# Optimization experiments

Measured on AMD Instinct MI355X. Metric: run time of the kernel, lower is better.

Reference implementation:

```python
import jax, jax.numpy as jnp
import numpy as np

D_MODEL = 1024
NUM_HEADS = 16
D_K = D_MODEL // NUM_HEADS
NEG = jnp.float32(-1e9)  # finite stand-in for -inf to keep softmax NaN-free on fully masked rows


def setup_inputs() -> dict:
    key = jax.random.key(0)
    ks = jax.random.split(key, 7)
    B, N_q, N_kv = 2, 2048, 2048
    x = jax.random.normal(ks[0], (B, N_q, D_MODEL), dtype=jnp.float32)
    K = jax.random.normal(ks[1], (B, NUM_HEADS, N_kv, D_K), dtype=jnp.float32)
    V = jax.random.normal(ks[2], (B, NUM_HEADS, N_kv, D_K), dtype=jnp.float32)
    # pad masks: True = keep. Ensure first kv position is always valid.
    kv_pad_mask = jax.random.uniform(ks[3], (B, 1, 1, N_kv)) > 0.1
    kv_pad_mask = kv_pad_mask.at[..., 0].set(True)
    q_pad_mask = jax.random.uniform(ks[4], (B, 1, N_q, 1)) > 0.1
    # params (torch Linear, bias=False); stored as [in, out] so y = x @ W
    Wq = jax.random.normal(ks[5], (D_MODEL, D_MODEL), dtype=jnp.float32) / np.sqrt(D_MODEL)
    Wo = jax.random.normal(ks[6], (D_MODEL, D_MODEL), dtype=jnp.float32) / np.sqrt(D_MODEL)
    return {"x": x, "K": K, "V": V, "Wq": Wq, "Wo": Wo,
            "kv_pad_mask": kv_pad_mask, "q_pad_mask": q_pad_mask}


def reference(x, K, V, Wq, Wo, kv_pad_mask, q_pad_mask):
    B, N_q, D = x.shape
    H, d_k = NUM_HEADS, D_K
    # Q projection and split into heads: [B, H, N_q, d_k]
    Q = (x @ Wq).reshape(B, N_q, H, d_k).transpose(0, 2, 1, 3)
    scores = jnp.einsum('bhqd,bhkd->bhqk', Q, K) / np.sqrt(d_k).astype(np.float32)
    keep = q_pad_mask & kv_pad_mask  # broadcast to [B,1,N_q,N_kv]
    scores = jnp.where(keep, scores, NEG)
    probs = jax.nn.softmax(scores, axis=-1)
    attn = jnp.einsum('bhqk,bhkd->bhqd', probs, V)  # [B,H,N_q,d_k]
    attn = attn.transpose(0, 2, 1, 3).reshape(B, N_q, H * d_k)
    return attn @ Wo
```

## Files before the change

kernel.cpp:

```cpp
#include <hip/hip_runtime.h>
#include <hip/hip_bf16.h>
#include <stdint.h>

typedef __hip_bfloat16 bf16;
typedef __attribute__((ext_vector_type(8))) short short8;
typedef __attribute__((ext_vector_type(4))) short s16x4;
typedef __attribute__((ext_vector_type(4))) float floatx4;

#define MFMA16(a, b, c) __builtin_amdgcn_mfma_f32_16x16x32_bf16(a, b, c, 0, 0, 0)

__device__ __forceinline__ void async_lds16(const void* g, void* l) {
  __builtin_amdgcn_global_load_lds((__attribute__((address_space(1))) const void*)g,
                                   (__attribute__((address_space(3))) void*)l, 16, 0, 0);
}

__device__ __forceinline__ unsigned rne2(float a, float b) {
  unsigned ua = __float_as_uint(a), ub = __float_as_uint(b);
  ua = ua + 0x7FFFu + ((ua >> 16) & 1u);
  ub = ub + 0x7FFFu + ((ub >> 16) & 1u);
  return (ua >> 16) | (ub & 0xFFFF0000u);
}

__global__ __launch_bounds__(256) void prep_k(const float* __restrict__ x, bf16* __restrict__ xb,
                                              const float* __restrict__ Kf, bf16* __restrict__ Kb,
                                              const float* __restrict__ Wq, bf16* __restrict__ WqT,
                                              const float* __restrict__ Wo, bf16* __restrict__ WoT,
                                              const float* __restrict__ V, bf16* __restrict__ VTb,
                                              const int* __restrict__ kvm, const int* __restrict__ qm,
                                              float* __restrict__ kvB, float* __restrict__ qB) {
  __shared__ float tile[64][65];
  int bid = blockIdx.x, tid = threadIdx.x;
  if (bid < 8192) {
    const float* s; bf16* d; int g = bid;
    if (g < 4096) { s = x; d = xb; } else { s = Kf; d = Kb; g -= 4096; }
    int i = (g * 256 + tid) * 4;
    float4 v = *(const float4*)(s + i);
    uint2 o = {rne2(v.x, v.y), rne2(v.z, v.w)};
    *(uint2*)(d + i) = o;
    return;
  }
  if (bid < 9744 - 16) {
    const float* s; bf16* d; int r0, c0, R, C;
    if (bid < 8704) {
      int idx = bid - 8192;
      s = (idx >> 8) ? Wo : Wq; d = (idx >> 8) ? WoT : WqT;
      int rem = idx & 255;
      r0 = (rem & 15) * 64; c0 = (rem >> 4) * 64; R = 1024; C = 1024;
    } else {
      int idx = bid - 8704;
      int m = idx >> 5;
      s = V + (size_t)m * 2048 * 64; d = VTb + (size_t)m * 2048 * 64;
      r0 = (idx & 31) * 64; c0 = 0; R = 2048; C = 64;
    }
    int tr = tid >> 2, tg = tid & 3;
#pragma unroll
    for (int k = 0; k < 4; ++k) {
      int col = tg * 16 + k * 4;
      float4 v = *(const float4*)(s + (size_t)(r0 + tr) * C + c0 + col);
      tile[tr][col] = v.x; tile[tr][col + 1] = v.y;
      tile[tr][col + 2] = v.z; tile[tr][col + 3] = v.w;
    }
    __syncthreads();
    int orow = tid >> 2, ch = tid & 3;
    bf16* drow = d + (size_t)(c0 + orow) * R + r0;
    uint4 w0, w1;
    w0.x = rne2(tile[ch * 8 + 0][orow], tile[ch * 8 + 1][orow]);
    w0.y = rne2(tile[ch * 8 + 2][orow], tile[ch * 8 + 3][orow]);
    w0.z = rne2(tile[ch * 8 + 4][orow], tile[ch * 8 + 5][orow]);
    w0.w = rne2(tile[ch * 8 + 6][orow], tile[ch * 8 + 7][orow]);
    w1.x = rne2(tile[32 + ch * 8 + 0][orow], tile[32 + ch * 8 + 1][orow]);
    w1.y = rne2(tile[32 + ch * 8 + 2][orow], tile[32 + ch * 8 + 3][orow]);
    w1.z = rne2(tile[32 + ch * 8 + 4][orow], tile[32 + ch * 8 + 5][orow]);
    w1.w = rne2(tile[32 + ch * 8 + 6][orow], tile[32 + ch * 8 + 7][orow]);
    *(uint4*)(drow + ch * 8) = w0;
    *(uint4*)(drow + 32 + ch * 8) = w1;
    return;
  }
  int i = (bid - (9744 - 16)) * 256 + tid;
  kvB[i] = kvm[i] ? 0.0f : -3000.0f;
  qB[i]  = qm[i]  ? 0.0f : -3000.0f;
}

__device__ __forceinline__ void storeC(bf16* C, size_t i, float v) { C[i] = __float2bfloat16(v); }
__device__ __forceinline__ void storeC(float* C, size_t i, float v) { C[i] = v; }

template <typename OT>
__global__ __launch_bounds__(256) void gemm_bt_k(const bf16* __restrict__ A,
                                                 const bf16* __restrict__ BT,
                                                 OT* __restrict__ C,
                                                 int M, int N, int K, float scale) {
  __shared__ __align__(16) bf16 As[64 * 64];
  __shared__ __align__(16) bf16 Bs[64 * 64];
  int tid = threadIdx.x;
  int wave = tid >> 6, lane = tid & 63;
  int quad = lane >> 4, lm = lane & 15;
  int wm = wave >> 1, wn = wave & 1;
  int row0 = blockIdx.y * 64, col0 = blockIdx.x * 64;

  floatx4 acc[2][2];
#pragma unroll
  for (int mt = 0; mt < 2; ++mt)
#pragma unroll
    for (int nt = 0; nt < 2; ++nt) acc[mt][nt] = (floatx4){0.f, 0.f, 0.f, 0.f};

  for (int k0 = 0; k0 < K; k0 += 64) {
    __syncthreads();
#pragma unroll
    for (int ch = 0; ch < 2; ++ch) {
      int e = (wave * 2 + ch) * 512 + lane * 8;
      int r = e >> 6, c16 = (e & 63) >> 3;
      int sc = (c16 ^ (r & 7)) * 8;
      async_lds16(A + (size_t)(row0 + r) * K + k0 + sc, &As[(wave * 2 + ch) * 512]);
    }
#pragma unroll
    for (int ch = 0; ch < 2; ++ch) {
      int e = (wave * 2 + ch) * 512 + lane * 8;
      int r = e >> 6, c16 = (e & 63) >> 3;
      int sc = (c16 ^ (r & 7)) * 8;
      async_lds16(BT + (size_t)(col0 + r) * K + k0 + sc, &Bs[(wave * 2 + ch) * 512]);
    }
    __syncthreads();
    int sw = lm & 7;
#pragma unroll
    for (int ks = 0; ks < 64; ks += 32) {
      short8 af[2], bfr[2];
#pragma unroll
      for (int mt = 0; mt < 2; ++mt) {
        int R = wm * 32 + mt * 16 + lm;
        af[mt] = *(const short8*)&As[R * 64 + ((((ks >> 3) + quad) ^ sw) * 8)];
      }
#pragma unroll
      for (int nt = 0; nt < 2; ++nt) {
        int R = wn * 32 + nt * 16 + lm;
        bfr[nt] = *(const short8*)&Bs[R * 64 + ((((ks >> 3) + quad) ^ sw) * 8)];
      }
#pragma unroll
      for (int mt = 0; mt < 2; ++mt)
#pragma unroll
        for (int nt = 0; nt < 2; ++nt)
          acc[mt][nt] = MFMA16(af[mt], bfr[nt], acc[mt][nt]);
    }
  }
#pragma unroll
  for (int mt = 0; mt < 2; ++mt)
#pragma unroll
    for (int nt = 0; nt < 2; ++nt)
#pragma unroll
      for (int j = 0; j < 4; ++j) {
        int rr = row0 + wm * 32 + mt * 16 + quad * 4 + j;
        int cc = col0 + wn * 32 + nt * 16 + lm;
        storeC(C, (size_t)rr * N + cc, acc[mt][nt][j] * scale);
      }
}

__global__ __launch_bounds__(256, 4) void attn_k(const bf16* __restrict__ Q,
                                                 const bf16* __restrict__ Km,
                                                 const bf16* __restrict__ VT,
                                                 const float* __restrict__ qB,
                                                 const float* __restrict__ kvB,
                                                 bf16* __restrict__ O) {
  const float TINY = 9.313225746154785e-10f;
  __shared__ __align__(16) bf16 Ks[64 * 64];
  __shared__ __align__(16) bf16 Vs[64 * 64];
  __shared__ __align__(16) float kvBs[2048];

  int tid = threadIdx.x;
  int wave = tid >> 6, lane = tid & 63;
  int quad = lane >> 4, lm = lane & 15;
  int qb = blockIdx.x, h = blockIdx.y, b = blockIdx.z;
  int q0 = qb * 64 + wave * 16;

  const bf16* kbase = Km + (size_t)(b * 16 + h) * 2048 * 64;
  const bf16* vbase = VT + (size_t)(b * 16 + h) * 64 * 2048;
  const float* kvBb = kvB + b * 2048;

#pragma unroll
  for (int c = 0; c < 2; ++c)
    async_lds16(kvBb + (wave * 2 + c) * 256 + lane * 4, &kvBs[(wave * 2 + c) * 256]);

  short8 aq0, aq1;
  float qbias;
  {
    const bf16* qp = Q + (size_t)(b * 2048 + q0 + lm) * 1024 + h * 64 + quad * 8;
    aq0 = *(const short8*)qp;
    aq1 = *(const short8*)(qp + 32);
    qbias = qB[b * 2048 + q0 + lm];
  }

  short8 ones;
#pragma unroll
  for (int i = 0; i < 8; ++i) ones[i] = (short)0x3F80;

  floatx4 o_acc[4];
  floatx4 l_acc = (floatx4){0.f, 0.f, 0.f, 0.f};
#pragma unroll
  for (int t = 0; t < 4; ++t) o_acc[t] = (floatx4){0.f, 0.f, 0.f, 0.f};

  union S8U { short8 s8; s16x4 h[2]; unsigned u[4]; };

  for (int kv0 = 0; kv0 < 2048; kv0 += 64) {
    __syncthreads();
#pragma unroll
    for (int c = 0; c < 2; ++c) {
      int o = (wave * 2 + c) * 1024 + lane * 16;
      int r = o >> 7;
      int g16 = (o >> 4) & 7;
      int sc = ((g16 ^ (r & 7)) * 8);
      async_lds16(kbase + (size_t)(kv0 + r) * 64 + sc, &Ks[(wave * 2 + c) * 512]);
      async_lds16(vbase + (size_t)r * 2048 + kv0 + sc, &Vs[(wave * 2 + c) * 512]);
    }
    __syncthreads();

    S8U pf[2];
#pragma unroll
    for (int t = 0; t < 4; ++t) {
      int R = t * 16 + lm, sw = lm & 7;
      short8 kf0 = *(const short8*)&Ks[R * 64 + ((quad ^ sw) * 8)];
      short8 kf1 = *(const short8*)&Ks[R * 64 + (((quad + 4) ^ sw) * 8)];
      floatx4 z = *(const floatx4*)&kvBs[kv0 + t * 16 + quad * 4];
#pragma unroll
      for (int j = 0; j < 4; ++j) z[j] += qbias;
      z = MFMA16(kf0, aq0, z);
      z = MFMA16(kf1, aq1, z);
      float p0 = __builtin_amdgcn_exp2f(z[0]) + TINY;
      float p1 = __builtin_amdgcn_exp2f(z[1]) + TINY;
      float p2 = __builtin_amdgcn_exp2f(z[2]) + TINY;
      float p3 = __builtin_amdgcn_exp2f(z[3]) + TINY;
      pf[t >> 1].u[(t & 1) * 2 + 0] = rne2(p0, p1);
      pf[t >> 1].u[(t & 1) * 2 + 1] = rne2(p2, p3);
    }
#pragma unroll
    for (int t = 0; t < 4; ++t) {
      int D = t * 16 + lm, sw = lm & 7;
      int hoff = (quad & 1) * 4, qh = quad >> 1;
      S8U vf0, vf1;
      vf0.h[0] = *(const s16x4*)&Vs[D * 64 + (((0 + qh) ^ sw) * 8) + hoff];
      vf0.h[1] = *(const s16x4*)&Vs[D * 64 + (((2 + qh) ^ sw) * 8) + hoff];
      vf1.h[0] = *(const s16x4*)&Vs[D * 64 + (((4 + qh) ^ sw) * 8) + hoff];
      vf1.h[1] = *(const s16x4*)&Vs[D * 64 + (((6 + qh) ^ sw) * 8) + hoff];
      o_acc[t] = MFMA16(vf0.s8, pf[0].s8, o_acc[t]);
      o_acc[t] = MFMA16(vf1.s8, pf[1].s8, o_acc[t]);
    }
    l_acc = MFMA16(ones, pf[0].s8, l_acc);
    l_acc = MFMA16(ones, pf[1].s8, l_acc);
  }
  float rl = 1.0f / l_acc[0];
  bf16* orow = O + (size_t)(b * 2048 + q0 + lm) * 1024 + h * 64;
#pragma unroll
  for (int t = 0; t < 4; ++t) {
    uint2 ov = {rne2(o_acc[t][0] * rl, o_acc[t][1] * rl),
                rne2(o_acc[t][2] * rl, o_acc[t][3] * rl)};
    *(uint2*)(orow + t * 16 + quad * 4) = ov;
  }
}

extern "C" void kernel_launch(void* const* d_in, const int* in_sizes, int n_in,
                              void* d_out, int out_size, void* d_ws, size_t ws_size,
                              hipStream_t stream) {
  const float* x  = (const float*)d_in[0];
  const float* K  = (const float*)d_in[1];
  const float* V  = (const float*)d_in[2];
  const float* Wq = (const float*)d_in[3];
  const float* Wo = (const float*)d_in[4];
  const int* kvm  = (const int*)d_in[5];
  const int* qm   = (const int*)d_in[6];

  char* w = (char*)d_ws;
  bf16* xb    = (bf16*)(w);
  bf16* attnb = xb;
  bf16* Qb    = (bf16*)(w + (8u << 20));
  bf16* Kb    = (bf16*)(w + (16u << 20));
  bf16* VTb   = (bf16*)(w + (24u << 20));
  bf16* WqT   = (bf16*)(w + (32u << 20));
  bf16* WoT   = (bf16*)(w + (34u << 20));
  float* qB   = (float*)(w + (36u << 20));
  float* kvB  = (float*)(w + (36u << 20) + 16384);

  const float SCL2 = 0.18033688011112042f;

  prep_k<<<9744, 256, 0, stream>>>(x, xb, K, Kb, Wq, WqT, Wo, WoT, V, VTb, kvm, qm, kvB, qB);
  gemm_bt_k<bf16><<<dim3(16, 64), 256, 0, stream>>>(xb, WqT, Qb, 4096, 1024, 1024, SCL2);
  attn_k<<<dim3(32, 16, 2), 256, 0, stream>>>(Qb, Kb, VTb, qB, kvB, attnb);
  gemm_bt_k<float><<<dim3(16, 64), 256, 0, stream>>>(attnb, WoT, (float*)d_out, 4096, 1024, 1024, 1.0f);
}
```

Baseline: 204.6 us.

## Double-buffer LDS tiles in GEMM and attention kernels with async prefetch

Both the projection GEMM and the attention kernel now keep two LDS buffers for their input tiles and issue the async global-to-LDS loads for the next tile before computing on the current one. Explicit s_waitcnt on vmcnt and raw s_barriers replace the old sync-load-sync pattern. The kv bias preload in attention switches from async LDS loads to plain vector loads plus stores. This is meant to hide global memory latency behind MFMA work, at the cost of doubled LDS use, which may lower occupancy for attn_k (launch bounds 4). It also relies on hand-encoded waitcnt immediates being correct.

```diff
diff --git a/kernel.cpp b/kernel.cpp
--- a/kernel.cpp
+++ b/kernel.cpp
@@ -8,6 +8,8 @@
 typedef __attribute__((ext_vector_type(4))) float floatx4;
 
 #define MFMA16(a, b, c) __builtin_amdgcn_mfma_f32_16x16x32_bf16(a, b, c, 0, 0, 0)
+#define WAIT_VM4 3956
+#define WAIT_VM0 3952
 
 __device__ __forceinline__ void async_lds16(const void* g, void* l) {
   __builtin_amdgcn_global_load_lds((__attribute__((address_space(1))) const void*)g,
@@ -89,8 +91,8 @@
                                                  const bf16* __restrict__ BT,
                                                  OT* __restrict__ C,
                                                  int M, int N, int K, float scale) {
-  __shared__ __align__(16) bf16 As[64 * 64];
-  __shared__ __align__(16) bf16 Bs[64 * 64];
+  __shared__ __align__(16) bf16 As[2][64 * 64];
+  __shared__ __align__(16) bf16 Bs[2][64 * 64];
   int tid = threadIdx.x;
   int wave = tid >> 6, lane = tid & 63;
   int quad = lane >> 4, lm = lane & 15;
@@ -103,23 +105,30 @@
 #pragma unroll
     for (int nt = 0; nt < 2; ++nt) acc[mt][nt] = (floatx4){0.f, 0.f, 0.f, 0.f};
 
-  for (int k0 = 0; k0 < K; k0 += 64) {
-    __syncthreads();
+  auto stageAB = [&](int buf, int k0) {
 #pragma unroll
     for (int ch = 0; ch < 2; ++ch) {
       int e = (wave * 2 + ch) * 512 + lane * 8;
       int r = e >> 6, c16 = (e & 63) >> 3;
       int sc = (c16 ^ (r & 7)) * 8;
-      async_lds16(A + (size_t)(row0 + r) * K + k0 + sc, &As[(wave * 2 + ch) * 512]);
-    }
-#pragma unroll
-    for (int ch = 0; ch < 2; ++ch) {
-      int e = (wave * 2 + ch) * 512 + lane * 8;
-      int r = e >> 6, c16 = (e & 63) >> 3;
-      int sc = (c16 ^ (r & 7)) * 8;
-      async_lds16(BT + (size_t)(col0 + r) * K + k0 + sc, &Bs[(wave * 2 + ch) * 512]);
-    }
-    __syncthreads();
+      async_lds16(A + (size_t)(row0 + r) * K + k0 + sc, &As[buf][(wave * 2 + ch) * 512]);
+      async_lds16(BT + (size_t)(col0 + r) * K + k0 + sc, &Bs[buf][(wave * 2 + ch) * 512]);
+    }
+  };
+
+  int niter = K >> 6;
+  stageAB(0, 0);
+  for (int i = 0; i < niter; ++i) {
+    __builtin_amdgcn_s_barrier();
+    if (i + 1 < niter) {
+      stageAB((i + 1) & 1, (i + 1) << 6);
+      __builtin_amdgcn_s_waitcnt(WAIT_VM4);
+    } else {
+      __builtin_amdgcn_s_waitcnt(WAIT_VM0);
+    }
+    __builtin_amdgcn_s_barrier();
+    const bf16* Ac = As[i & 1];
+    const bf16* Bc = Bs[i & 1];
     int sw = lm & 7;
 #pragma unroll
     for (int ks = 0; ks < 64; ks += 32) {
@@ -127,12 +136,12 @@
 #pragma unroll
       for (int mt = 0; mt < 2; ++mt) {
         int R = wm * 32 + mt * 16 + lm;
-        af[mt] = *(const short8*)&As[R * 64 + ((((ks >> 3) + quad) ^ sw) * 8)];
+        af[mt] = *(const short8*)&Ac[R * 64 + ((((ks >> 3) + quad) ^ sw) * 8)];
       }
 #pragma unroll
       for (int nt = 0; nt < 2; ++nt) {
         int R = wn * 32 + nt * 16 + lm;
-        bfr[nt] = *(const short8*)&Bs[R * 64 + ((((ks >> 3) + quad) ^ sw) * 8)];
+        bfr[nt] = *(const short8*)&Bc[R * 64 + ((((ks >> 3) + quad) ^ sw) * 8)];
       }
 #pragma unroll
       for (int mt = 0; mt < 2; ++mt)
@@ -160,8 +169,8 @@
                                                  const float* __restrict__ kvB,
                                                  bf16* __restrict__ O) {
   const float TINY = 9.313225746154785e-10f;
-  __shared__ __align__(16) bf16 Ks[64 * 64];
-  __shared__ __align__(16) bf16 Vs[64 * 64];
+  __shared__ __align__(16) bf16 Ks[2][64 * 64];
+  __shared__ __align__(16) bf16 Vs[2][64 * 64];
   __shared__ __align__(16) float kvBs[2048];
 
   int tid = threadIdx.x;
@@ -174,9 +183,12 @@
   const bf16* vbase = VT + (size_t)(b * 16 + h) * 64 * 2048;
   const float* kvBb = kvB + b * 2048;
 
-#pragma unroll
-  for (int c = 0; c < 2; ++c)
-    async_lds16(kvBb + (wave * 2 + c) * 256 + lane * 4, &kvBs[(wave * 2 + c) * 256]);
+  {
+    float4 v0 = *(const float4*)(kvBb + tid * 8);
+    float4 v1 = *(const float4*)(kvBb + tid * 8 + 4);
+    *(float4*)&kvBs[tid * 8] = v0;
+    *(float4*)&kvBs[tid * 8 + 4] = v1;
+  }
 
   short8 aq0, aq1;
   float qbias;
@@ -198,25 +210,39 @@
 
   union S8U { short8 s8; s16x4 h[2]; unsigned u[4]; };
 
-  for (int kv0 = 0; kv0 < 2048; kv0 += 64) {
-    __syncthreads();
+  auto stageKV = [&](int buf, int kv0) {
 #pragma unroll
     for (int c = 0; c < 2; ++c) {
       int o = (wave * 2 + c) * 1024 + lane * 16;
       int r = o >> 7;
       int g16 = (o >> 4) & 7;
       int sc = ((g16 ^ (r & 7)) * 8);
-      async_lds16(kbase + (size_t)(kv0 + r) * 64 + sc, &Ks[(wave * 2 + c) * 512]);
-      async_lds16(vbase + (size_t)r * 2048 + kv0 + sc, &Vs[(wave * 2 + c) * 512]);
-    }
-    __syncthreads();
+      async_lds16(kbase + (size_t)(kv0 + r) * 64 + sc, &Ks[buf][(wave * 2 + c) * 512]);
+      async_lds16(vbase + (size_t)r * 2048 + kv0 + sc, &Vs[buf][(wave * 2 + c) * 512]);
+    }
+  };
+
+  __syncthreads();
+  stageKV(0, 0);
+  for (int i = 0; i < 32; ++i) {
+    int kv0 = i * 64;
+    __builtin_amdgcn_s_barrier();
+    if (i + 1 < 32) {
+      stageKV((i + 1) & 1, kv0 + 64);
+      __builtin_amdgcn_s_waitcnt(WAIT_VM4);
+    } else {
+      __builtin_amdgcn_s_waitcnt(WAIT_VM0);
+    }
+    __builtin_amdgcn_s_barrier();
+    const bf16* Kc = Ks[i & 1];
+    const bf16* Vc = Vs[i & 1];
 
     S8U pf[2];
 #pragma unroll
     for (int t = 0; t < 4; ++t) {
       int R = t * 16 + lm, sw = lm & 7;
-      short8 kf0 = *(const short8*)&Ks[R * 64 + ((quad ^ sw) * 8)];
-      short8 kf1 = *(const short8*)&Ks[R * 64 + (((quad + 4) ^ sw) * 8)];
+      short8 kf0 = *(const short8*)&Kc[R * 64 + ((quad ^ sw) * 8)];
+      short8 kf1 = *(const short8*)&Kc[R * 64 + (((quad + 4) ^ sw) * 8)];
       floatx4 z = *(const floatx4*)&kvBs[kv0 + t * 16 + quad * 4];
 #pragma unroll
       for (int j = 0; j < 4; ++j) z[j] += qbias;
@@ -234,10 +260,10 @@
       int D = t * 16 + lm, sw = lm & 7;
       int hoff = (quad & 1) * 4, qh = quad >> 1;
       S8U vf0, vf1;
-      vf0.h[0] = *(const s16x4*)&Vs[D * 64 + (((0 + qh) ^ sw) * 8) + hoff];
-      vf0.h[1] = *(const s16x4*)&Vs[D * 64 + (((2 + qh) ^ sw) * 8) + hoff];
-      vf1.h[0] = *(const s16x4*)&Vs[D * 64 + (((4 + qh) ^ sw) * 8) + hoff];
-      vf1.h[1] = *(const s16x4*)&Vs[D * 64 + (((6 + qh) ^ sw) * 8) + hoff];
+      vf0.h[0] = *(const s16x4*)&Vc[D * 64 + (((0 + qh) ^ sw) * 8) + hoff];
+      vf0.h[1] = *(const s16x4*)&Vc[D * 64 + (((2 + qh) ^ sw) * 8) + hoff];
+      vf1.h[0] = *(const s16x4*)&Vc[D * 64 + (((4 + qh) ^ sw) * 8) + hoff];
+      vf1.h[1] = *(const s16x4*)&Vc[D * 64 + (((6 + qh) ^ sw) * 8) + hoff];
       o_acc[t] = MFMA16(vf0.s8, pf[0].s8, o_acc[t]);
       o_acc[t] = MFMA16(vf1.s8, pf[1].s8, o_acc[t]);
     }
```

Measured after the change: 200.8 us. Within noise of the previous version (-1.9%).
